# Kernel optimization log

Measured on AMD Instinct MI355X. Metric: run time of the kernel, lower is better.

Reference implementation:

```python
import jax, jax.numpy as jnp
import numpy as np
from math import sqrt

L_LAYERS = 4
VOCAB = 32000
D = 1024
H = 16
HD = D // H
FFN = 4096
B = 4
LT = 1024
LS = 1024
NEG = -1e9
EPS = 1e-6


def rms_norm(x, g):
    ms = jnp.mean(x * x, axis=-1, keepdims=True)
    return x / jnp.sqrt(ms + EPS) * g


def attention(q_in, kv_in, wq, wk, wv, wo, mask=None):
    # q_in: [B,Lq,D], kv_in: [B,Lk,D]; weights [D,D]
    Bq, Lq, _ = q_in.shape
    Lk = kv_in.shape[1]
    q = (q_in @ wq).reshape(Bq, Lq, H, HD).transpose(0, 2, 1, 3)
    k = (kv_in @ wk).reshape(Bq, Lk, H, HD).transpose(0, 2, 1, 3)
    v = (kv_in @ wv).reshape(Bq, Lk, H, HD).transpose(0, 2, 1, 3)
    scores = jnp.einsum('bhqd,bhkd->bhqk', q, k) / sqrt(HD)
    if mask is not None:
        scores = scores + mask  # [Lq,Lk] broadcast
    attn = jax.nn.softmax(scores, axis=-1)
    out = jnp.einsum('bhqk,bhkd->bhqd', attn, v)
    out = out.transpose(0, 2, 1, 3).reshape(Bq, Lq, D)
    return out @ wo


def setup_inputs() -> dict:
    key = jax.random.key(0)
    ks = jax.random.split(key, 20)
    s = 0.02
    inp = {
        'input_ids': jax.random.randint(ks[0], (B, LT), 0, VOCAB),
        'memory': jax.random.normal(ks[1], (B, LS, D), dtype=jnp.float32),
        'embed': jax.random.normal(ks[2], (VOCAB, D), dtype=jnp.float32) * s,
        'sa_g': jnp.ones((L_LAYERS, D), dtype=jnp.float32),
        'sa_wq': jax.random.normal(ks[3], (L_LAYERS, D, D), dtype=jnp.float32) * s,
        'sa_wk': jax.random.normal(ks[4], (L_LAYERS, D, D), dtype=jnp.float32) * s,
        'sa_wv': jax.random.normal(ks[5], (L_LAYERS, D, D), dtype=jnp.float32) * s,
        'sa_wo': jax.random.normal(ks[6], (L_LAYERS, D, D), dtype=jnp.float32) * s,
        'ca_g': jnp.ones((L_LAYERS, D), dtype=jnp.float32),
        'ca_wq': jax.random.normal(ks[7], (L_LAYERS, D, D), dtype=jnp.float32) * s,
        'ca_wk': jax.random.normal(ks[8], (L_LAYERS, D, D), dtype=jnp.float32) * s,
        'ca_wv': jax.random.normal(ks[9], (L_LAYERS, D, D), dtype=jnp.float32) * s,
        'ca_wo': jax.random.normal(ks[10], (L_LAYERS, D, D), dtype=jnp.float32) * s,
        'mlp_g': jnp.ones((L_LAYERS, D), dtype=jnp.float32),
        'w1': jax.random.normal(ks[11], (L_LAYERS, D, FFN), dtype=jnp.float32) * s,
        'w2': jax.random.normal(ks[12], (L_LAYERS, FFN, D), dtype=jnp.float32) * s,
        'final_g': jnp.ones((D,), dtype=jnp.float32),
    }
    return inp


def reference(input_ids, memory, embed, sa_g, sa_wq, sa_wk, sa_wv, sa_wo,
              ca_g, ca_wq, ca_wk, ca_wv, ca_wo, mlp_g, w1, w2, final_g):
    Lt = input_ids.shape[1]
    causal = jnp.where(jnp.triu(jnp.ones((Lt, Lt), dtype=bool), k=1), NEG, 0.0).astype(jnp.float32)
    x = embed[input_ids]  # [B,Lt,D]
    for i in range(L_LAYERS):
        h = rms_norm(x, sa_g[i])
        x = x + attention(h, h, sa_wq[i], sa_wk[i], sa_wv[i], sa_wo[i], mask=causal)
        h = rms_norm(x, ca_g[i])
        x = x + attention(h, memory, ca_wq[i], ca_wk[i], ca_wv[i], ca_wo[i])
        h = rms_norm(x, mlp_g[i])
        x = x + jax.nn.relu(h @ w1[i]) @ w2[i]
    return rms_norm(x, final_g)
```

## Files before the change

### kernel.cpp

```cpp
#include <hip/hip_runtime.h>
#include <stdint.h>

#define NLAYERS 4
#define D      1024
#define H      16
#define HD     64
#define FFN    4096
#define BATCH  4
#define LT     1024
#define LS     1024
#define BT     (BATCH*LT)

typedef unsigned short u16;
typedef long long ll;

typedef short  short8 __attribute__((ext_vector_type(8)));
typedef float  f32x4  __attribute__((ext_vector_type(4)));

typedef __attribute__((address_space(1))) void as1_void;
typedef __attribute__((address_space(3))) void as3_void;

__device__ __forceinline__ float bf2f(u16 u) {
    unsigned int x = ((unsigned int)u) << 16;
    return __builtin_bit_cast(float, x);
}
__device__ __forceinline__ u16 f2bf(float f) {
    unsigned int x = __builtin_bit_cast(unsigned int, f);
    x += 0x7fffu + ((x >> 16) & 1u);
    return (u16)(x >> 16);
}

__device__ __forceinline__ void load16_to_lds(const void* g, void* l) {
    __builtin_amdgcn_global_load_lds((as1_void*)(void*)g, (as3_void*)l, 16, 0, 0);
}

__global__ void probe_kernel(const unsigned int* __restrict__ g, int* __restrict__ flag)
{
    if (threadIdx.x == 0) *flag = (*g == 0x3F803F80u) ? 0 : 1;
}

__global__ __launch_bounds__(256) void gemm_bt(
    const u16* __restrict__ A, const u16* __restrict__ Bt,
    void* __restrict__ Cout,
    int K, int lda, int ldb, int ldc,
    ll strideA, ll strideB, ll strideC,
    int Nvalid, int mode)
{
    __shared__ u16 sA[128 * 32];
    __shared__ u16 sB[128 * 32];

    const int tid  = threadIdx.x;
    const int wave = tid >> 6;
    const int lane = tid & 63;
    const int wm   = wave >> 1;
    const int wn   = wave & 1;
    const int quad = lane >> 4;
    const int l16  = lane & 15;
    const int bm = blockIdx.y, bn = blockIdx.x;
    const ll  z  = blockIdx.z;

    const u16* Ab = A + z * strideA;
    const u16* Bb = Bt + z * strideB;

    f32x4 acc[4][4];
#pragma unroll
    for (int i = 0; i < 4; ++i)
#pragma unroll
        for (int j = 0; j < 4; ++j) acc[i][j] = (f32x4){0.f, 0.f, 0.f, 0.f};

    const int i0 = wave * 64 + lane;
    const int i1 = 256 + i0;
    const int rA0 = i0 >> 2, ke0 = (i0 & 3) * 8;
    const int rA1 = i1 >> 2, ke1 = (i1 & 3) * 8;
    u16* lA0 = &sA[(wave * 64) * 8];
    u16* lA1 = &sA[(256 + wave * 64) * 8];
    u16* lB0 = &sB[(wave * 64) * 8];
    u16* lB1 = &sB[(256 + wave * 64) * 8];

    const u16* gA0 = Ab + (ll)(bm * 128 + rA0) * lda + ke0;
    const u16* gA1 = Ab + (ll)(bm * 128 + rA1) * lda + ke1;
    const u16* gB0 = Bb + (ll)(bn * 128 + rA0) * ldb + ke0;
    const u16* gB1 = Bb + (ll)(bn * 128 + rA1) * ldb + ke1;

    for (int kt = 0; kt < K; kt += 32) {
        __syncthreads();
        load16_to_lds(gA0 + kt, lA0);
        load16_to_lds(gA1 + kt, lA1);
        load16_to_lds(gB0 + kt, lB0);
        load16_to_lds(gB1 + kt, lB1);
        __syncthreads();

        short8 af[4], bfv[4];
#pragma unroll
        for (int mi = 0; mi < 4; ++mi) {
            int r = wm * 64 + mi * 16 + l16;
            af[mi] = *(const short8*)&sA[r * 32 + quad * 8];
        }
#pragma unroll
        for (int ni = 0; ni < 4; ++ni) {
            int n = wn * 64 + ni * 16 + l16;
            bfv[ni] = *(const short8*)&sB[n * 32 + quad * 8];
        }
#pragma unroll
        for (int mi = 0; mi < 4; ++mi)
#pragma unroll
            for (int ni = 0; ni < 4; ++ni)
                acc[mi][ni] = __builtin_amdgcn_mfma_f32_16x16x32_bf16(
                    af[mi], bfv[ni], acc[mi][ni], 0, 0, 0);
    }

    if (mode == 3) {
        float* O = (float*)Cout;
#pragma unroll
        for (int mi = 0; mi < 4; ++mi) {
#pragma unroll
            for (int r = 0; r < 4; ++r) {
                int row = bm * 128 + wm * 64 + mi * 16 + quad * 4 + r;
                ll base = z * strideC + (ll)row * ldc;
#pragma unroll
                for (int ni = 0; ni < 4; ++ni) {
                    int col = bn * 128 + wn * 64 + ni * 16 + l16;
                    if (col < Nvalid) atomicAdd(&O[base + col], acc[mi][ni][r]);
                }
            }
        }
    } else {
        u16* O = (u16*)Cout;
#pragma unroll
        for (int mi = 0; mi < 4; ++mi) {
#pragma unroll
            for (int r = 0; r < 4; ++r) {
                int row = bm * 128 + wm * 64 + mi * 16 + quad * 4 + r;
                ll base = z * strideC + (ll)row * ldc;
#pragma unroll
                for (int ni = 0; ni < 4; ++ni) {
                    int col = bn * 128 + wn * 64 + ni * 16 + l16;
                    if (col < Nvalid) {
                        float v = acc[mi][ni][r];
                        if (mode == 1) v = fmaxf(v, 0.f);
                        O[base + col] = f2bf(v);
                    }
                }
            }
        }
    }
}

#define FA_PAD 136

__global__ __launch_bounds__(256) void flash_attn(
    const u16* __restrict__ Qp, int q_ld,
    const u16* __restrict__ Kp, int k_ld,
    const u16* __restrict__ Vt,
    u16* __restrict__ Op, int o_ld, int causal)
{
    __shared__ u16 sK[2 * 128 * 32];
    __shared__ u16 sV[4 * 64 * 32];
    __shared__ u16 sP[128 * FA_PAD];
    __shared__ float pmax[2 * 128];
    __shared__ float psum[2 * 128];

    const int tid  = threadIdx.x;
    const int wave = tid >> 6, lane = tid & 63;
    const int wm = wave >> 1, wn = wave & 1;
    const int quad = lane >> 4, l16 = lane & 15;
    const int bm = blockIdx.x;
    const int z  = blockIdx.y;
    const int b = z >> 4, h = z & 15;

    const u16* Qb = Qp + (ll)(b * LT) * q_ld + h * HD;
    const u16* Kb = Kp + (ll)(b * LS) * k_ld + h * HD;
    const u16* Vb = Vt + (ll)z * HD * LS;

    u16* sQ = sP;
#pragma unroll
    for (int j = 0; j < 4; ++j) {
        int i = wave * 256 + j * 64 + lane;
        int ks = i >> 9, n = (i >> 2) & 127, c = i & 3;
        const u16* g = Qb + (ll)(bm * 128 + n) * q_ld + ks * 32 + c * 8;
        load16_to_lds(g, (char*)sQ + (wave * 256 + j * 64) * 16);
    }
    __syncthreads();
    short8 afq[4][2];
#pragma unroll
    for (int mi = 0; mi < 4; ++mi)
#pragma unroll
        for (int ks = 0; ks < 2; ++ks)
            afq[mi][ks] = *(const short8*)&sQ[ks * 4096 + (wm * 64 + mi * 16 + l16) * 32 + quad * 8];
    __syncthreads();

    float m_s[4][4], l_s[4][4];
    f32x4 Oacc[4][2];
#pragma unroll
    for (int mi = 0; mi < 4; ++mi)
#pragma unroll
        for (int r = 0; r < 4; ++r) { m_s[mi][r] = -1e30f; l_s[mi][r] = 0.f; }
#pragma unroll
    for (int mi = 0; mi < 4; ++mi)
#pragma unroll
        for (int di = 0; di < 2; ++di) Oacc[mi][di] = (f32x4){0.f, 0.f, 0.f, 0.f};

    const int n_kt = causal ? (bm + 1) : (LS / 128);

    for (int kt = 0; kt < n_kt; ++kt) {
#pragma unroll
        for (int j = 0; j < 4; ++j) {
            int i = wave * 256 + j * 64 + lane;
            int ks = i >> 9, n = (i >> 2) & 127, c = i & 3;
            const u16* g = Kb + (ll)(kt * 128 + n) * k_ld + ks * 32 + c * 8;
            load16_to_lds(g, (char*)sK + (wave * 256 + j * 64) * 16);
        }
#pragma unroll
        for (int j = 0; j < 4; ++j) {
            int i = wave * 256 + j * 64 + lane;
            int kk = i >> 8, d = (i >> 2) & 63, c = i & 3;
            const u16* g = Vb + (ll)d * LS + kt * 128 + kk * 32 + c * 8;
            load16_to_lds(g, (char*)sV + (wave * 256 + j * 64) * 16);
        }
        __syncthreads();

        f32x4 s[4][4];
#pragma unroll
        for (int mi = 0; mi < 4; ++mi)
#pragma unroll
            for (int ni = 0; ni < 4; ++ni) s[mi][ni] = (f32x4){0.f, 0.f, 0.f, 0.f};
#pragma unroll
        for (int ks = 0; ks < 2; ++ks) {
            short8 bk[4];
#pragma unroll
            for (int ni = 0; ni < 4; ++ni)
                bk[ni] = *(const short8*)&sK[ks * 4096 + (wn * 64 + ni * 16 + l16) * 32 + quad * 8];
#pragma unroll
            for (int mi = 0; mi < 4; ++mi)
#pragma unroll
                for (int ni = 0; ni < 4; ++ni)
                    s[mi][ni] = __builtin_amdgcn_mfma_f32_16x16x32_bf16(
                        afq[mi][ks], bk[ni], s[mi][ni], 0, 0, 0);
        }

        float pm[4][4];
#pragma unroll
        for (int mi = 0; mi < 4; ++mi)
#pragma unroll
            for (int r = 0; r < 4; ++r) pm[mi][r] = -1e30f;
#pragma unroll
        for (int mi = 0; mi < 4; ++mi)
#pragma unroll
            for (int ni = 0; ni < 4; ++ni)
#pragma unroll
                for (int r = 0; r < 4; ++r) {
                    float v = s[mi][ni][r] * 0.125f;
                    if (causal) {
                        int rowg = bm * 128 + wm * 64 + mi * 16 + quad * 4 + r;
                        int colg = kt * 128 + wn * 64 + ni * 16 + l16;
                        if (colg > rowg) v = -1e30f;
                    }
                    s[mi][ni][r] = v;
                    pm[mi][r] = fmaxf(pm[mi][r], v);
                }
#pragma unroll
        for (int off = 1; off < 16; off <<= 1)
#pragma unroll
            for (int mi = 0; mi < 4; ++mi)
#pragma unroll
                for (int r = 0; r < 4; ++r)
                    pm[mi][r] = fmaxf(pm[mi][r], __shfl_xor(pm[mi][r], off));
        if (l16 == 0)
#pragma unroll
            for (int mi = 0; mi < 4; ++mi)
#pragma unroll
                for (int r = 0; r < 4; ++r)
                    pmax[wn * 128 + wm * 64 + mi * 16 + quad * 4 + r] = pm[mi][r];
        __syncthreads();

        float alpha[4][4], ps[4][4];
#pragma unroll
        for (int mi = 0; mi < 4; ++mi)
#pragma unroll
            for (int r = 0; r < 4; ++r) {
                int row = wm * 64 + mi * 16 + quad * 4 + r;
                float rm = fmaxf(pmax[row], pmax[128 + row]);
                float mnew = fmaxf(m_s[mi][r], rm);
                alpha[mi][r] = __expf(m_s[mi][r] - mnew);
                m_s[mi][r] = mnew;
                ps[mi][r] = 0.f;
            }
#pragma unroll
        for (int mi = 0; mi < 4; ++mi)
#pragma unroll
            for (int ni = 0; ni < 4; ++ni)
#pragma unroll
                for (int r = 0; r < 4; ++r) {
                    float pv = __expf(s[mi][ni][r] - m_s[mi][r]);
                    ps[mi][r] += pv;
                    sP[(wm * 64 + mi * 16 + quad * 4 + r) * FA_PAD + wn * 64 + ni * 16 + l16] = f2bf(pv);
                }
#pragma unroll
        for (int off = 1; off < 16; off <<= 1)
#pragma unroll
            for (int mi = 0; mi < 4; ++mi)
#pragma unroll
                for (int r = 0; r < 4; ++r)
                    ps[mi][r] += __shfl_xor(ps[mi][r], off);
        if (l16 == 0)
#pragma unroll
            for (int mi = 0; mi < 4; ++mi)
#pragma unroll
                for (int r = 0; r < 4; ++r)
                    psum[wn * 128 + wm * 64 + mi * 16 + quad * 4 + r] = ps[mi][r];
        __syncthreads();

#pragma unroll
        for (int mi = 0; mi < 4; ++mi)
#pragma unroll
            for (int r = 0; r < 4; ++r) {
                int row = wm * 64 + mi * 16 + quad * 4 + r;
                l_s[mi][r] = l_s[mi][r] * alpha[mi][r] + psum[row] + psum[128 + row];
            }
#pragma unroll
        for (int mi = 0; mi < 4; ++mi)
#pragma unroll
            for (int di = 0; di < 2; ++di)
#pragma unroll
                for (int r = 0; r < 4; ++r) Oacc[mi][di][r] *= alpha[mi][r];
#pragma unroll
        for (int kk = 0; kk < 4; ++kk) {
            short8 ap[4], bv[2];
#pragma unroll
            for (int mi = 0; mi < 4; ++mi)
                ap[mi] = *(const short8*)&sP[(wm * 64 + mi * 16 + l16) * FA_PAD + kk * 32 + quad * 8];
#pragma unroll
            for (int di = 0; di < 2; ++di)
                bv[di] = *(const short8*)&sV[kk * 2048 + (wn * 32 + di * 16 + l16) * 32 + quad * 8];
#pragma unroll
            for (int mi = 0; mi < 4; ++mi)
#pragma unroll
                for (int di = 0; di < 2; ++di)
                    Oacc[mi][di] = __builtin_amdgcn_mfma_f32_16x16x32_bf16(
                        ap[mi], bv[di], Oacc[mi][di], 0, 0, 0);
        }
        __syncthreads();
    }

#pragma unroll
    for (int mi = 0; mi < 4; ++mi)
#pragma unroll
        for (int di = 0; di < 2; ++di)
#pragma unroll
            for (int r = 0; r < 4; ++r) {
                int rowg = bm * 128 + wm * 64 + mi * 16 + quad * 4 + r;
                int col  = h * HD + wn * 32 + di * 16 + l16;
                Op[(ll)(b * LT + rowg) * o_ld + col] = f2bf(Oacc[mi][di][r] / l_s[mi][r]);
            }
}

__global__ __launch_bounds__(256) void transpose_any(
    const void* __restrict__ inb, ll elem_off, u16* __restrict__ out,
    int in_stride, int out_stride, const int* __restrict__ flagp)
{
    __shared__ u16 t[32][33];
    const int fl = *flagp;
    int bk = blockIdx.x * 32;
    int bn = blockIdx.y * 32;
    int c  = threadIdx.x & 31;
    int r0 = threadIdx.x >> 5;
#pragma unroll
    for (int i = 0; i < 4; ++i) {
        int r = r0 + i * 8;
        ll idx = elem_off + (ll)(bk + r) * in_stride + bn + c;
        t[r][c] = fl ? f2bf(((const float*)inb)[idx]) : ((const u16*)inb)[idx];
    }
    __syncthreads();
#pragma unroll
    for (int i = 0; i < 4; ++i) {
        int r = r0 + i * 8;
        out[(ll)(bn + r) * out_stride + bk + c] = t[c][r];
    }
}

__global__ __launch_bounds__(256) void trans3_kernel(
    const void* __restrict__ s0, const void* __restrict__ s1, const void* __restrict__ s2,
    ll elem_off, u16* __restrict__ dst, const int* __restrict__ flagp)
{
    __shared__ u16 t[32][33];
    const int fl = *flagp;
    int zz = blockIdx.z;
    const void* src = (zz == 0) ? s0 : (zz == 1) ? s1 : s2;
    u16* out = dst + (ll)zz * D * D;
    int bk = blockIdx.x * 32, bn = blockIdx.y * 32;
    int c = threadIdx.x & 31, r0 = threadIdx.x >> 5;
#pragma unroll
    for (int i = 0; i < 4; ++i) {
        int r = r0 + i * 8;
        ll idx = elem_off + (ll)(bk + r) * D + bn + c;
        t[r][c] = fl ? f2bf(((const float*)src)[idx]) : ((const u16*)src)[idx];
    }
    __syncthreads();
#pragma unroll
    for (int i = 0; i < 4; ++i) {
        int r = r0 + i * 8;
        out[(ll)(bn + r) * D + bk + c] = t[c][r];
    }
}

__global__ __launch_bounds__(256) void transpose_v_kernel(
    const u16* __restrict__ V, int v_ld, u16* __restrict__ Vt)
{
    __shared__ u16 t[32][33];
    int z = blockIdx.z;
    int b = z >> 4, h = z & 15;
    const u16* in = V + (ll)b * LT * v_ld + h * HD;
    u16* out = Vt + (ll)z * HD * LS;
    int bt = blockIdx.x * 32;
    int bd = blockIdx.y * 32;
    int c  = threadIdx.x & 31;
    int r0 = threadIdx.x >> 5;
#pragma unroll
    for (int i = 0; i < 4; ++i) {
        int r = r0 + i * 8;
        t[r][c] = in[(ll)(bt + r) * v_ld + bd + c];
    }
    __syncthreads();
#pragma unroll
    for (int i = 0; i < 4; ++i) {
        int r = r0 + i * 8;
        out[(ll)(bd + r) * LS + bt + c] = t[c][r];
    }
}

__global__ __launch_bounds__(256) void convert_memory(
    const void* __restrict__ mem, u16* __restrict__ out, const int* __restrict__ flagp)
{
    const int fl = *flagp;
    ll i = (ll)blockIdx.x * 1024 + threadIdx.x * 4;
#pragma unroll
    for (int j = 0; j < 4; ++j)
        out[i + j] = fl ? f2bf(((const float*)mem)[i + j]) : ((const u16*)mem)[i + j];
}

__global__ __launch_bounds__(256) void embed_kernel(
    const int* __restrict__ ids, const void* __restrict__ emb, float* __restrict__ x,
    const int* __restrict__ flagp)
{
    const int fl = *flagp;
    ll row = blockIdx.x;
    int id = ids[row];
    float* xr = x + row * D;
    int j = threadIdx.x * 4;
#pragma unroll
    for (int i = 0; i < 4; ++i) {
        ll idx = (ll)id * D + j + i;
        xr[j + i] = fl ? ((const float*)emb)[idx] : bf2f(((const u16*)emb)[idx]);
    }
}

__global__ __launch_bounds__(256) void rmsnorm_kernel(
    const float* __restrict__ x, const void* __restrict__ gb, ll g_off,
    void* __restrict__ out, const int* __restrict__ flagp, int is_final)
{
    __shared__ float red[4];
    const int fl = *flagp;
    ll row = blockIdx.x;
    const float* xr = x + row * D;
    int tid = threadIdx.x;
    float4 v = ((const float4*)xr)[tid];
    float s = v.x * v.x + v.y * v.y + v.z * v.z + v.w * v.w;
#pragma unroll
    for (int o = 32; o; o >>= 1) s += __shfl_xor(s, o);
    if ((tid & 63) == 0) red[tid >> 6] = s;
    __syncthreads();
    s = red[0] + red[1] + red[2] + red[3];
    float inv = rsqrtf(s * (1.0f / D) + 1e-6f);
    int j = tid * 4;
    float e[4] = {v.x, v.y, v.z, v.w};
#pragma unroll
    for (int i = 0; i < 4; ++i) {
        ll gi = g_off + j + i;
        float g = fl ? ((const float*)gb)[gi] : bf2f(((const u16*)gb)[gi]);
        float val = e[i] * inv * g;
        if (is_final && fl) ((float*)out)[row * D + j + i] = val;
        else                ((u16*)out)[row * D + j + i] = f2bf(val);
    }
}

extern "C" void kernel_launch(void* const* d_in, const int* in_sizes, int n_in,
                              void* d_out, int out_size, void* d_ws, size_t ws_size,
                              hipStream_t stream)
{
    (void)in_sizes; (void)n_in; (void)out_size; (void)ws_size;

    const int*  ids    = (const int*)d_in[0];
    const void* memory = d_in[1];
    const void* embed  = d_in[2];
    const void* sa_g   = d_in[3];
    const void* sa_wq  = d_in[4];
    const void* sa_wk  = d_in[5];
    const void* sa_wv  = d_in[6];
    const void* sa_wo  = d_in[7];
    const void* ca_g   = d_in[8];
    const void* ca_wq  = d_in[9];
    const void* ca_wk  = d_in[10];
    const void* ca_wv  = d_in[11];
    const void* ca_wo  = d_in[12];
    const void* mlp_g  = d_in[13];
    const void* w1     = d_in[14];
    const void* w2     = d_in[15];
    const void* final_g= d_in[16];

    char* p = (char*)d_ws;
    auto alloc = [&](size_t bytes) -> void* {
        void* r = (void*)p;
        p += (bytes + 255) & ~(size_t)255;
        return r;
    };
    int*   flag   = (int*)alloc(256);
    u16*   wt_qkv = (u16*)alloc((size_t)3 * D * D * 2);
    u16*   wt_q   = wt_qkv;
    u16*   wt_kv  = wt_qkv + (size_t)D * D;
    u16*   wt_o   = (u16*)alloc((size_t)D * D * 2);
    u16*   wt1    = (u16*)alloc((size_t)FFN * D * 2);
    u16*   wt2    = (u16*)alloc((size_t)D * FFN * 2);
    float* x      = (float*)alloc((size_t)BT * D * 4);
    u16*   h      = (u16*)alloc((size_t)BT * D * 2);
    u16*   memb   = (u16*)alloc((size_t)BT * D * 2);
    u16*   vt     = (u16*)alloc((size_t)BATCH * H * HD * LS * 2);
    u16*   ob     = (u16*)alloc((size_t)BT * D * 2);
    u16*   smid   = (u16*)alloc((size_t)BT * FFN * 2);
    u16*   qkvb   = smid;
    u16*   mid    = smid;

    probe_kernel<<<1, 64, 0, stream>>>((const unsigned int*)final_g, flag);

    auto gemm = [&](const u16* A, const u16* Bt, void* C,
                    int M, int Npad, int K, int lda, int ldb, int ldc,
                    ll sA, ll sB, ll sC, int batch, int mode) {
        dim3 grid(Npad / 128, M / 128, batch);
        gemm_bt<<<grid, 256, 0, stream>>>(A, Bt, C, K, lda, ldb, ldc,
                                          sA, sB, sC, Npad, mode);
    };

    embed_kernel<<<BT, 256, 0, stream>>>(ids, embed, x, flag);
    convert_memory<<<BT * D / 1024, 256, 0, stream>>>(memory, memb, flag);

    for (int il = 0; il < NLAYERS; ++il) {
        const ll wOff = (ll)il * D * D;

        trans3_kernel<<<dim3(D/32, D/32, 3), 256, 0, stream>>>(
            sa_wq, sa_wk, sa_wv, wOff, wt_qkv, flag);
        transpose_any<<<dim3(D/32, D/32), 256, 0, stream>>>(sa_wo, wOff, wt_o, D, D, flag);
        rmsnorm_kernel<<<BT, 256, 0, stream>>>(x, sa_g, (ll)il * D, h, flag, 0);
        gemm(h, wt_qkv, qkvb, BT, 3 * D, D, D, D, 3 * D, 0, 0, 0, 1, 0);
        transpose_v_kernel<<<dim3(LT/32, HD/32, BATCH*H), 256, 0, stream>>>(qkvb + 2 * D, 3 * D, vt);
        flash_attn<<<dim3(LT/128, BATCH*H), 256, 0, stream>>>(
            qkvb, 3 * D, qkvb + D, 3 * D, vt, ob, D, 1);
        gemm(ob, wt_o, x, BT, D, 512, D, D, D, 512, 512, 0, 2, 3);

        trans3_kernel<<<dim3(D/32, D/32, 3), 256, 0, stream>>>(
            ca_wq, ca_wk, ca_wv, wOff, wt_qkv, flag);
        transpose_any<<<dim3(D/32, D/32), 256, 0, stream>>>(ca_wo, wOff, wt_o, D, D, flag);
        rmsnorm_kernel<<<BT, 256, 0, stream>>>(x, ca_g, (ll)il * D, h, flag, 0);
        gemm(h, wt_q, qkvb, BT, D, D, D, D, 3 * D, 0, 0, 0, 1, 0);
        gemm(memb, wt_kv, qkvb + D, BT, 2 * D, D, D, D, 3 * D, 0, 0, 0, 1, 0);
        transpose_v_kernel<<<dim3(LT/32, HD/32, BATCH*H), 256, 0, stream>>>(qkvb + 2 * D, 3 * D, vt);
        flash_attn<<<dim3(LT/128, BATCH*H), 256, 0, stream>>>(
            qkvb, 3 * D, qkvb + D, 3 * D, vt, ob, D, 0);
        gemm(ob, wt_o, x, BT, D, 512, D, D, D, 512, 512, 0, 2, 3);

        transpose_any<<<dim3(D/32, FFN/32), 256, 0, stream>>>(w1, (ll)il * D * FFN, wt1, FFN, D, flag);
        transpose_any<<<dim3(FFN/32, D/32), 256, 0, stream>>>(w2, (ll)il * FFN * D, wt2, D, FFN, flag);
        rmsnorm_kernel<<<BT, 256, 0, stream>>>(x, mlp_g, (ll)il * D, h, flag, 0);
        gemm(h, wt1, mid, BT, FFN, D, D, D, FFN, 0, 0, 0, 1, 1);
        gemm(mid, wt2, x, BT, D, 2048, FFN, FFN, D, 2048, 2048, 0, 2, 3);
    }

    rmsnorm_kernel<<<BT, 256, 0, stream>>>(x, final_g, 0, d_out, flag, 1);
}
```

Measured before the change: 2.701 ms.

## Restructure flash attention to per-wave row ownership and raise split-K for output GEMMs

Flash attention now gives each wave a full 32-row strip across all 128 keys, so row max and row sum no longer go through LDS and two block barriers per tile disappear. The row sum is computed with an extra MFMA against a ones vector, exp2 with a pre-folded log2e scale replaces expf, and masking runs only on the diagonal tile. The K and P buffers share one LDS region and the kernel asks for 3 blocks per CU. Separately, the wo and w2 projection GEMMs use split-K of 4 instead of 2, trading more atomic or accumulate passes for more parallel blocks.

```diff
diff --git a/kernel.cpp b/kernel.cpp
--- a/kernel.cpp
+++ b/kernel.cpp
@@ -146,24 +146,24 @@
     }
 }
 
-#define FA_PAD 136
-
-__global__ __launch_bounds__(256) void flash_attn(
+#define FA_PAD 132
+
+__global__ __launch_bounds__(256, 3) void flash_attn(
     const u16* __restrict__ Qp, int q_ld,
     const u16* __restrict__ Kp, int k_ld,
     const u16* __restrict__ Vt,
     u16* __restrict__ Op, int o_ld, int causal)
 {
-    __shared__ u16 sK[2 * 128 * 32];
+    __shared__ u16 uni[128 * FA_PAD];
     __shared__ u16 sV[4 * 64 * 32];
-    __shared__ u16 sP[128 * FA_PAD];
-    __shared__ float pmax[2 * 128];
-    __shared__ float psum[2 * 128];
+
+    u16* sK = uni;
+    u16* sP = uni;
 
     const int tid  = threadIdx.x;
     const int wave = tid >> 6, lane = tid & 63;
-    const int wm = wave >> 1, wn = wave & 1;
     const int quad = lane >> 4, l16 = lane & 15;
+    const int rw   = wave * 32;
     const int bm = blockIdx.x;
     const int z  = blockIdx.y;
     const int b = z >> 4, h = z & 15;
@@ -172,33 +172,36 @@
     const u16* Kb = Kp + (ll)(b * LS) * k_ld + h * HD;
     const u16* Vb = Vt + (ll)z * HD * LS;
 
-    u16* sQ = sP;
 #pragma unroll
     for (int j = 0; j < 4; ++j) {
         int i = wave * 256 + j * 64 + lane;
         int ks = i >> 9, n = (i >> 2) & 127, c = i & 3;
-        const u16* g = Qb + (ll)(bm * 128 + n) * q_ld + ks * 32 + c * 8;
-        load16_to_lds(g, (char*)sQ + (wave * 256 + j * 64) * 16);
+        load16_to_lds(Qb + (ll)(bm * 128 + n) * q_ld + ks * 32 + c * 8,
+                      (char*)uni + (wave * 256 + j * 64) * 16);
     }
     __syncthreads();
-    short8 afq[4][2];
-#pragma unroll
-    for (int mi = 0; mi < 4; ++mi)
+    short8 afq[2][2];
+#pragma unroll
+    for (int mi = 0; mi < 2; ++mi)
 #pragma unroll
         for (int ks = 0; ks < 2; ++ks)
-            afq[mi][ks] = *(const short8*)&sQ[ks * 4096 + (wm * 64 + mi * 16 + l16) * 32 + quad * 8];
+            afq[mi][ks] = *(const short8*)&uni[ks * 4096 + (rw + mi * 16 + l16) * 32 + quad * 8];
     __syncthreads();
 
-    float m_s[4][4], l_s[4][4];
-    f32x4 Oacc[4][2];
-#pragma unroll
-    for (int mi = 0; mi < 4; ++mi)
-#pragma unroll
-        for (int r = 0; r < 4; ++r) { m_s[mi][r] = -1e30f; l_s[mi][r] = 0.f; }
-#pragma unroll
-    for (int mi = 0; mi < 4; ++mi)
-#pragma unroll
-        for (int di = 0; di < 2; ++di) Oacc[mi][di] = (f32x4){0.f, 0.f, 0.f, 0.f};
+    float m_s[2][4];
+    f32x4 Oacc[2][4], Ol[2];
+#pragma unroll
+    for (int mi = 0; mi < 2; ++mi) {
+#pragma unroll
+        for (int r = 0; r < 4; ++r) m_s[mi][r] = -1e30f;
+#pragma unroll
+        for (int di = 0; di < 4; ++di) Oacc[mi][di] = (f32x4){0.f, 0.f, 0.f, 0.f};
+        Ol[mi] = (f32x4){0.f, 0.f, 0.f, 0.f};
+    }
+    const float c1 = 0.1803368801111204f;
+    short8 ones;
+#pragma unroll
+    for (int i = 0; i < 8; ++i) ones[i] = (short)0x3F80;
 
     const int n_kt = causal ? (bm + 1) : (LS / 128);
 
@@ -207,150 +210,128 @@
         for (int j = 0; j < 4; ++j) {
             int i = wave * 256 + j * 64 + lane;
             int ks = i >> 9, n = (i >> 2) & 127, c = i & 3;
-            const u16* g = Kb + (ll)(kt * 128 + n) * k_ld + ks * 32 + c * 8;
-            load16_to_lds(g, (char*)sK + (wave * 256 + j * 64) * 16);
+            load16_to_lds(Kb + (ll)(kt * 128 + n) * k_ld + ks * 32 + c * 8,
+                          (char*)sK + (wave * 256 + j * 64) * 16);
         }
 #pragma unroll
         for (int j = 0; j < 4; ++j) {
             int i = wave * 256 + j * 64 + lane;
             int kk = i >> 8, d = (i >> 2) & 63, c = i & 3;
-            const u16* g = Vb + (ll)d * LS + kt * 128 + kk * 32 + c * 8;
-            load16_to_lds(g, (char*)sV + (wave * 256 + j * 64) * 16);
+            load16_to_lds(Vb + (ll)d * LS + kt * 128 + kk * 32 + c * 8,
+                          (char*)sV + (wave * 256 + j * 64) * 16);
         }
         __syncthreads();
 
-        f32x4 s[4][4];
-#pragma unroll
-        for (int mi = 0; mi < 4; ++mi)
-#pragma unroll
-            for (int ni = 0; ni < 4; ++ni) s[mi][ni] = (f32x4){0.f, 0.f, 0.f, 0.f};
-#pragma unroll
-        for (int ks = 0; ks < 2; ++ks) {
-            short8 bk[4];
-#pragma unroll
-            for (int ni = 0; ni < 4; ++ni)
-                bk[ni] = *(const short8*)&sK[ks * 4096 + (wn * 64 + ni * 16 + l16) * 32 + quad * 8];
-#pragma unroll
-            for (int mi = 0; mi < 4; ++mi)
-#pragma unroll
-                for (int ni = 0; ni < 4; ++ni)
-                    s[mi][ni] = __builtin_amdgcn_mfma_f32_16x16x32_bf16(
-                        afq[mi][ks], bk[ni], s[mi][ni], 0, 0, 0);
-        }
-
-        float pm[4][4];
-#pragma unroll
-        for (int mi = 0; mi < 4; ++mi)
+        f32x4 s[2][8];
+#pragma unroll
+        for (int mi = 0; mi < 2; ++mi)
+#pragma unroll
+            for (int ni = 0; ni < 8; ++ni) s[mi][ni] = (f32x4){0.f, 0.f, 0.f, 0.f};
+#pragma unroll
+        for (int ks = 0; ks < 2; ++ks)
+#pragma unroll
+            for (int nh = 0; nh < 2; ++nh) {
+                short8 bk[4];
+#pragma unroll
+                for (int nn = 0; nn < 4; ++nn)
+                    bk[nn] = *(const short8*)&sK[ks * 4096 + ((nh * 4 + nn) * 16 + l16) * 32 + quad * 8];
+#pragma unroll
+                for (int mi = 0; mi < 2; ++mi)
+#pragma unroll
+                    for (int nn = 0; nn < 4; ++nn)
+                        s[mi][nh * 4 + nn] = __builtin_amdgcn_mfma_f32_16x16x32_bf16(
+                            afq[mi][ks], bk[nn], s[mi][nh * 4 + nn], 0, 0, 0);
+            }
+        __syncthreads();
+
+        const int diag = causal && (kt == bm);
+        float pm[2][4];
+#pragma unroll
+        for (int mi = 0; mi < 2; ++mi)
 #pragma unroll
             for (int r = 0; r < 4; ++r) pm[mi][r] = -1e30f;
 #pragma unroll
-        for (int mi = 0; mi < 4; ++mi)
-#pragma unroll
-            for (int ni = 0; ni < 4; ++ni)
+        for (int mi = 0; mi < 2; ++mi)
+#pragma unroll
+            for (int ni = 0; ni < 8; ++ni)
 #pragma unroll
                 for (int r = 0; r < 4; ++r) {
-                    float v = s[mi][ni][r] * 0.125f;
-                    if (causal) {
-                        int rowg = bm * 128 + wm * 64 + mi * 16 + quad * 4 + r;
-                        int colg = kt * 128 + wn * 64 + ni * 16 + l16;
-                        if (colg > rowg) v = -1e30f;
+                    float t = s[mi][ni][r] * c1;
+                    if (diag) {
+                        int rowg = rw + mi * 16 + quad * 4 + r;
+                        int colg = ni * 16 + l16;
+                        if (colg > rowg) t = -1e30f;
                     }
-                    s[mi][ni][r] = v;
-                    pm[mi][r] = fmaxf(pm[mi][r], v);
+                    s[mi][ni][r] = t;
+                    pm[mi][r] = fmaxf(pm[mi][r], t);
                 }
 #pragma unroll
         for (int off = 1; off < 16; off <<= 1)
 #pragma unroll
-            for (int mi = 0; mi < 4; ++mi)
+            for (int mi = 0; mi < 2; ++mi)
 #pragma unroll
                 for (int r = 0; r < 4; ++r)
                     pm[mi][r] = fmaxf(pm[mi][r], __shfl_xor(pm[mi][r], off));
-        if (l16 == 0)
-#pragma unroll
-            for (int mi = 0; mi < 4; ++mi)
-#pragma unroll
-                for (int r = 0; r < 4; ++r)
-                    pmax[wn * 128 + wm * 64 + mi * 16 + quad * 4 + r] = pm[mi][r];
-        __syncthreads();
-
-        float alpha[4][4], ps[4][4];
-#pragma unroll
-        for (int mi = 0; mi < 4; ++mi)
+
+        float alpha[2][4];
+#pragma unroll
+        for (int mi = 0; mi < 2; ++mi)
 #pragma unroll
             for (int r = 0; r < 4; ++r) {
-                int row = wm * 64 + mi * 16 + quad * 4 + r;
-                float rm = fmaxf(pmax[row], pmax[128 + row]);
-                float mnew = fmaxf(m_s[mi][r], rm);
-                alpha[mi][r] = __expf(m_s[mi][r] - mnew);
+                float mnew = fmaxf(m_s[mi][r], pm[mi][r]);
+                alpha[mi][r] = __builtin_amdgcn_exp2f(m_s[mi][r] - mnew);
                 m_s[mi][r] = mnew;
-                ps[mi][r] = 0.f;
-            }
-#pragma unroll
-        for (int mi = 0; mi < 4; ++mi)
-#pragma unroll
-            for (int ni = 0; ni < 4; ++ni)
+            }
+#pragma unroll
+        for (int mi = 0; mi < 2; ++mi)
+#pragma unroll
+            for (int r = 0; r < 4; ++r) {
+#pragma unroll
+                for (int di = 0; di < 4; ++di) Oacc[mi][di][r] *= alpha[mi][r];
+                Ol[mi][r] *= alpha[mi][r];
+            }
+
+#pragma unroll
+        for (int mi = 0; mi < 2; ++mi)
+#pragma unroll
+            for (int ni = 0; ni < 8; ++ni)
 #pragma unroll
                 for (int r = 0; r < 4; ++r) {
-                    float pv = __expf(s[mi][ni][r] - m_s[mi][r]);
-                    ps[mi][r] += pv;
-                    sP[(wm * 64 + mi * 16 + quad * 4 + r) * FA_PAD + wn * 64 + ni * 16 + l16] = f2bf(pv);
+                    float pv = __builtin_amdgcn_exp2f(s[mi][ni][r] - m_s[mi][r]);
+                    sP[(rw + mi * 16 + quad * 4 + r) * FA_PAD + ni * 16 + l16] = f2bf(pv);
                 }
-#pragma unroll
-        for (int off = 1; off < 16; off <<= 1)
-#pragma unroll
-            for (int mi = 0; mi < 4; ++mi)
-#pragma unroll
-                for (int r = 0; r < 4; ++r)
-                    ps[mi][r] += __shfl_xor(ps[mi][r], off);
-        if (l16 == 0)
-#pragma unroll
-            for (int mi = 0; mi < 4; ++mi)
-#pragma unroll
-                for (int r = 0; r < 4; ++r)
-                    psum[wn * 128 + wm * 64 + mi * 16 + quad * 4 + r] = ps[mi][r];
-        __syncthreads();
-
-#pragma unroll
-        for (int mi = 0; mi < 4; ++mi)
-#pragma unroll
-            for (int r = 0; r < 4; ++r) {
-                int row = wm * 64 + mi * 16 + quad * 4 + r;
-                l_s[mi][r] = l_s[mi][r] * alpha[mi][r] + psum[row] + psum[128 + row];
-            }
-#pragma unroll
-        for (int mi = 0; mi < 4; ++mi)
-#pragma unroll
-            for (int di = 0; di < 2; ++di)
-#pragma unroll
-                for (int r = 0; r < 4; ++r) Oacc[mi][di][r] *= alpha[mi][r];
+
 #pragma unroll
         for (int kk = 0; kk < 4; ++kk) {
-            short8 ap[4], bv[2];
-#pragma unroll
-            for (int mi = 0; mi < 4; ++mi)
-                ap[mi] = *(const short8*)&sP[(wm * 64 + mi * 16 + l16) * FA_PAD + kk * 32 + quad * 8];
-#pragma unroll
-            for (int di = 0; di < 2; ++di)
-                bv[di] = *(const short8*)&sV[kk * 2048 + (wn * 32 + di * 16 + l16) * 32 + quad * 8];
-#pragma unroll
-            for (int mi = 0; mi < 4; ++mi)
-#pragma unroll
-                for (int di = 0; di < 2; ++di)
+            short8 ap[2], bv[4];
+#pragma unroll
+            for (int mi = 0; mi < 2; ++mi)
+                ap[mi] = *(const short8*)&sP[(rw + mi * 16 + l16) * FA_PAD + kk * 32 + quad * 8];
+#pragma unroll
+            for (int di = 0; di < 4; ++di)
+                bv[di] = *(const short8*)&sV[kk * 2048 + (di * 16 + l16) * 32 + quad * 8];
+#pragma unroll
+            for (int mi = 0; mi < 2; ++mi) {
+#pragma unroll
+                for (int di = 0; di < 4; ++di)
                     Oacc[mi][di] = __builtin_amdgcn_mfma_f32_16x16x32_bf16(
                         ap[mi], bv[di], Oacc[mi][di], 0, 0, 0);
+                Ol[mi] = __builtin_amdgcn_mfma_f32_16x16x32_bf16(
+                    ap[mi], ones, Ol[mi], 0, 0, 0);
+            }
         }
         __syncthreads();
     }
 
 #pragma unroll
-    for (int mi = 0; mi < 4; ++mi)
-#pragma unroll
-        for (int di = 0; di < 2; ++di)
+    for (int mi = 0; mi < 2; ++mi)
+#pragma unroll
+        for (int di = 0; di < 4; ++di)
 #pragma unroll
             for (int r = 0; r < 4; ++r) {
-                int rowg = bm * 128 + wm * 64 + mi * 16 + quad * 4 + r;
-                int col  = h * HD + wn * 32 + di * 16 + l16;
-                Op[(ll)(b * LT + rowg) * o_ld + col] = f2bf(Oacc[mi][di][r] / l_s[mi][r]);
+                int rowg = bm * 128 + rw + mi * 16 + quad * 4 + r;
+                int col  = h * HD + di * 16 + l16;
+                Op[(ll)(b * LT + rowg) * o_ld + col] = f2bf(Oacc[mi][di][r] / Ol[mi][r]);
             }
 }
 
@@ -553,7 +534,7 @@
         transpose_v_kernel<<<dim3(LT/32, HD/32, BATCH*H), 256, 0, stream>>>(qkvb + 2 * D, 3 * D, vt);
         flash_attn<<<dim3(LT/128, BATCH*H), 256, 0, stream>>>(
             qkvb, 3 * D, qkvb + D, 3 * D, vt, ob, D, 1);
-        gemm(ob, wt_o, x, BT, D, 512, D, D, D, 512, 512, 0, 2, 3);
+        gemm(ob, wt_o, x, BT, D, 256, D, D, D, 256, 256, 0, 4, 3);
 
         trans3_kernel<<<dim3(D/32, D/32, 3), 256, 0, stream>>>(
             ca_wq, ca_wk, ca_wv, wOff, wt_qkv, flag);
@@ -564,13 +545,13 @@
         transpose_v_kernel<<<dim3(LT/32, HD/32, BATCH*H), 256, 0, stream>>>(qkvb + 2 * D, 3 * D, vt);
         flash_attn<<<dim3(LT/128, BATCH*H), 256, 0, stream>>>(
             qkvb, 3 * D, qkvb + D, 3 * D, vt, ob, D, 0);
-        gemm(ob, wt_o, x, BT, D, 512, D, D, D, 512, 512, 0, 2, 3);
+        gemm(ob, wt_o, x, BT, D, 256, D, D, D, 256, 256, 0, 4, 3);
 
         transpose_any<<<dim3(D/32, FFN/32), 256, 0, stream>>>(w1, (ll)il * D * FFN, wt1, FFN, D, flag);
         transpose_any<<<dim3(FFN/32, D/32), 256, 0, stream>>>(w2, (ll)il * FFN * D, wt2, D, FFN, flag);
         rmsnorm_kernel<<<BT, 256, 0, stream>>>(x, mlp_g, (ll)il * D, h, flag, 0);
         gemm(h, wt1, mid, BT, FFN, D, D, D, FFN, 0, 0, 0, 1, 1);
-        gemm(mid, wt2, x, BT, D, 2048, FFN, FFN, D, 2048, 2048, 0, 2, 3);
+        gemm(mid, wt2, x, BT, D, 1024, FFN, FFN, D, 1024, 1024, 0, 4, 3);
     }
 
     rmsnorm_kernel<<<BT, 256, 0, stream>>>(x, final_g, 0, d_out, flag, 1);
```

Measured after the change: 2.719 ms. About the same (+0.7%).
